# Kernel tuning notes

Hardware: AMD Instinct MI355X
Metric: run time of the kernel (lower is better)

Reference implementation:

```python
import jax, jax.numpy as jnp
import numpy as np

B, T, D = 2, 2048, 2048
H, DH = 16, 128
FG = 5461
EPS = 1e-5
ROPE_BASE = 10000.0


def rmsnorm(x, w):
    rms = jax.lax.rsqrt(jnp.mean(x * x, axis=-1, keepdims=True) + EPS)
    return x * rms * w


def rotate_half(x):
    x1 = x[..., ::2]
    x2 = x[..., 1::2]
    return jnp.stack((-x2, x1), axis=-1).reshape(x.shape)


def rope_tables(t_len, dh, dtype):
    inv_freq = 1.0 / (ROPE_BASE ** (np.arange(0, dh, 2, dtype=np.float32) / dh))
    t = np.arange(t_len, dtype=np.float32)
    freqs = np.outer(t, inv_freq)                 # [T, dh/2]
    emb = np.repeat(freqs, 2, axis=-1)            # repeat_interleave -> [T, dh]
    return jnp.asarray(np.cos(emb), dtype), jnp.asarray(np.sin(emb), dtype)


def setup_inputs() -> dict:
    key = jax.random.key(0)
    ks = jax.random.split(key, 8)
    s_attn = 1.0 / np.sqrt(D)
    s_gate = 1.0 / np.sqrt(D)
    s_proj = 1.0 / np.sqrt(FG)
    return {
        "x": jax.random.normal(ks[0], (B, T, D), jnp.float32),
        "norm1_w": jnp.ones((D,), jnp.float32),
        "norm2_w": jnp.ones((D,), jnp.float32),
        "c_attn_w": jax.random.normal(ks[1], (3 * D, D), jnp.float32) * s_attn,
        "c_proj_w": jax.random.normal(ks[2], (D, D), jnp.float32) * s_attn,
        "c_gate_w": jax.random.normal(ks[3], (FG, D), jnp.float32) * s_gate,
        "c_val_w": jax.random.normal(ks[4], (FG, D), jnp.float32) * s_gate,
        "c_mlp_proj_w": jax.random.normal(ks[5], (D, FG), jnp.float32) * s_proj,
    }


def block(x, norm1_w, norm2_w, c_attn_w, c_proj_w, c_gate_w, c_val_w, c_mlp_proj_w):
    # ---- attention branch (pre-norm) ----
    h = rmsnorm(x, norm1_w)
    qkv = h @ c_attn_w.T                                   # [B,T,3D]
    qkv = qkv.reshape(B, T, 3, H, DH).transpose(2, 0, 3, 1, 4)
    q, k, v = qkv[0], qkv[1], qkv[2]                       # [B,H,T,DH]
    cos, sin = rope_tables(T, DH, x.dtype)                 # [T,DH]
    q = q * cos + rotate_half(q) * sin
    k = k * cos + rotate_half(k) * sin
    att = jnp.einsum("bhqd,bhkd->bhqk", q, k) * (1.0 / np.sqrt(DH))
    causal = jnp.tril(jnp.ones((T, T), bool))
    att = jnp.where(causal, att, -jnp.inf)
    att = jax.nn.softmax(att, axis=-1)
    y = jnp.einsum("bhqk,bhkd->bhqd", att, v)              # [B,H,T,DH]
    y = y.transpose(0, 2, 1, 3).reshape(B, T, D)
    x = x + y @ c_proj_w.T
    # ---- MLP branch (pre-norm, SwiGLU) ----
    h = rmsnorm(x, norm2_w)
    gate = jax.nn.silu(h @ c_gate_w.T)                     # [B,T,FG]
    val = h @ c_val_w.T
    x = x + (gate * val) @ c_mlp_proj_w.T
    return x


def reference(x, norm1_w, norm2_w, c_attn_w, c_proj_w, c_gate_w, c_val_w, c_mlp_proj_w):
    return block(x, norm1_w, norm2_w, c_attn_w, c_proj_w, c_gate_w, c_val_w, c_mlp_proj_w)
```

## Files before the change

### kernel.cpp

```cpp
#include <hip/hip_runtime.h>
#include <hip/hip_bf16.h>
#include <stdint.h>

typedef __bf16 bf16_t;
typedef __bf16 bf16x8 __attribute__((ext_vector_type(8)));
typedef float  f32x4  __attribute__((ext_vector_type(4)));

#define DEV __device__ __forceinline__

constexpr int   Bn = 2, Tn = 2048, Dn = 2048, Hn = 16, DHn = 128;
constexpr int   BTn = Bn * Tn;
constexpr int   TD3 = 3 * Dn;
constexpr int   FGn = 5461, FGPn = 5504;
constexpr float EPSf   = 1e-5f;
constexpr float LOG2E  = 1.4426950408889634f;
constexpr float ASCALE = 0.08838834764831845f;
constexpr float LN1E4  = 9.210340371976184f;

DEV void gld16(void* lds, const void* g) {
  __builtin_amdgcn_global_load_lds(
      (__attribute__((address_space(1))) void*)(void*)g,
      (__attribute__((address_space(3))) void*)lds, 16, 0, 0);
}

DEV bf16x8 dsr128(const bf16_t* p) {
  bf16x8 r;
  asm volatile("ds_read_b128 %0, %1"
               : "=v"(r)
               : "v"((const __attribute__((address_space(3))) bf16_t*)p));
  return r;
}

__global__ __launch_bounds__(256)
void rmsnorm_k(const float* __restrict__ x, const float* __restrict__ w,
               bf16_t* __restrict__ out) {
  const int row = blockIdx.x;
  const int tid = threadIdx.x;
  const float* xr = x + (size_t)row * Dn;
  float4 a = ((const float4*)xr)[tid * 2];
  float4 b = ((const float4*)xr)[tid * 2 + 1];
  float ss = a.x*a.x + a.y*a.y + a.z*a.z + a.w*a.w
           + b.x*b.x + b.y*b.y + b.z*b.z + b.w*b.w;
#pragma unroll
  for (int off = 32; off > 0; off >>= 1) ss += __shfl_xor(ss, off, 64);
  __shared__ float red[4];
  if ((tid & 63) == 0) red[tid >> 6] = ss;
  __syncthreads();
  float tot = red[0] + red[1] + red[2] + red[3];
  float rms = rsqrtf(tot * (1.0f / Dn) + EPSf);
  float4 wa = ((const float4*)w)[tid * 2];
  float4 wb = ((const float4*)w)[tid * 2 + 1];
  bf16x8 o;
  o[0] = (bf16_t)(a.x * rms * wa.x); o[1] = (bf16_t)(a.y * rms * wa.y);
  o[2] = (bf16_t)(a.z * rms * wa.z); o[3] = (bf16_t)(a.w * rms * wa.w);
  o[4] = (bf16_t)(b.x * rms * wb.x); o[5] = (bf16_t)(b.y * rms * wb.y);
  o[6] = (bf16_t)(b.z * rms * wb.z); o[7] = (bf16_t)(b.w * rms * wb.w);
  *(bf16x8*)&out[(size_t)row * Dn + tid * 8] = o;
}

__global__ __launch_bounds__(256)
void cvt_pad_k(const float* __restrict__ src, bf16_t* __restrict__ dst,
               int srcR, int srcC, int dstC, int n8) {
  int i = blockIdx.x * 256 + threadIdx.x;
  if (i >= n8) return;
  long base = (long)i * 8;
  int r = (int)(base / dstC);
  int c = (int)(base % dstC);
  bf16x8 o;
#pragma unroll
  for (int k = 0; k < 8; ++k) {
    int cc = c + k;
    float v = (r < srcR && cc < srcC) ? src[(size_t)r * srcC + cc] : 0.0f;
    o[k] = (bf16_t)v;
  }
  *(bf16x8*)&dst[base] = o;
}

__global__ __launch_bounds__(256)
void reduce_k(float* __restrict__ out, const bf16_t* __restrict__ P0,
              const bf16_t* __restrict__ P1) {
  int i = blockIdx.x * 256 + threadIdx.x;
  bf16x8 p0 = *(const bf16x8*)&P0[(size_t)i * 8];
  bf16x8 p1 = *(const bf16x8*)&P1[(size_t)i * 8];
  float4 o0 = ((const float4*)out)[i * 2];
  float4 o1 = ((const float4*)out)[i * 2 + 1];
  o0.x += (float)p0[0] + (float)p1[0];
  o0.y += (float)p0[1] + (float)p1[1];
  o0.z += (float)p0[2] + (float)p1[2];
  o0.w += (float)p0[3] + (float)p1[3];
  o1.x += (float)p0[4] + (float)p1[4];
  o1.y += (float)p0[5] + (float)p1[5];
  o1.z += (float)p0[6] + (float)p1[6];
  o1.w += (float)p0[7] + (float)p1[7];
  ((float4*)out)[i * 2]     = o0;
  ((float4*)out)[i * 2 + 1] = o1;
}

template<int EPI>
__global__ __launch_bounds__(512, 2)
void gemm256(const bf16_t* __restrict__ A, const bf16_t* __restrict__ W,
             void* Cp, const void* Ep, int M, int N, int K, int ldc, int nby) {
  __shared__ __align__(128) bf16_t As[4][256 * 32];
  __shared__ __align__(128) bf16_t Bs[4][256 * 32];
  const int tid = threadIdx.x;
  const int lane = tid & 63, w = tid >> 6;
  const int wm = w >> 2, wn = w & 3;
  const int g = lane >> 4, q = lane & 15;

  const int nwg = gridDim.x;
  const int cpx = nwg >> 3;
  const int nid = (blockIdx.x & 7) * cpx + (blockIdx.x >> 3);
  const int bx = nid / nby, by = nid % nby;
  const int row0 = by * 256, col0 = bx * 256;

  f32x4 acc[8][4] = {};

  const bf16_t* Asrc[2];
  const bf16_t* Wsrc[2];
  int aoff[2];
#pragma unroll
  for (int i = 0; i < 2; ++i) {
    int line = i * 64 + (tid >> 3);
    int val  = (tid & 7) ^ (line & 7);
    int r    = (val >> 2) * 128 + line;
    int c    = val & 3;
    Asrc[i] = A + (size_t)(row0 + r) * K + c * 8;
    Wsrc[i] = W + (size_t)(col0 + r) * K + c * 8;
    aoff[i] = i * 8192 + w * 1024;
  }

  int offA[8], offB[4];
#pragma unroll
  for (int m = 0; m < 8; ++m) {
    int r = wm * 128 + m * 16 + q;
    offA[m] = (r & 127) * 128 + ((((r >> 7) * 4 + g) ^ (r & 7)) * 16);
  }
#pragma unroll
  for (int n = 0; n < 4; ++n) {
    int r = wn * 64 + n * 16 + q;
    offB[n] = (r & 127) * 128 + ((((r >> 7) * 4 + g) ^ (r & 7)) * 16);
  }

  const int NT = K >> 5;
  auto stage_full = [&](int T) {
    const int slot = T & 3, kk = T * 32;
#pragma unroll
    for (int i = 0; i < 2; ++i) {
      gld16((char*)As[slot] + aoff[i], Asrc[i] + kk);
      gld16((char*)Bs[slot] + aoff[i], Wsrc[i] + kk);
    }
  };

  bf16x8 af[8], bfr[4];

  auto step = [&](int T, bool do_stage, int waitsel) {
    const char* as_ = (const char*)As[T & 3];
    const char* bs_ = (const char*)Bs[T & 3];
#pragma unroll
    for (int m = 0; m < 8; ++m) af[m] = dsr128((const bf16_t*)(as_ + offA[m]));
#pragma unroll
    for (int n = 0; n < 4; ++n) bfr[n] = dsr128((const bf16_t*)(bs_ + offB[n]));
    if (do_stage) stage_full(T + 3);
    asm volatile("s_waitcnt lgkmcnt(0)" ::: "memory");
    __builtin_amdgcn_sched_barrier(0);
    __builtin_amdgcn_s_setprio(1);
#pragma unroll
    for (int m = 0; m < 8; ++m)
#pragma unroll
      for (int n = 0; n < 4; ++n)
        acc[m][n] = __builtin_amdgcn_mfma_f32_16x16x32_bf16(af[m], bfr[n], acc[m][n], 0, 0, 0);
    __builtin_amdgcn_s_setprio(0);
    __builtin_amdgcn_sched_barrier(0);
    if (waitsel == 2)      asm volatile("s_waitcnt vmcnt(8)" ::: "memory");
    else if (waitsel == 1) asm volatile("s_waitcnt vmcnt(4)" ::: "memory");
    else if (waitsel == 0) asm volatile("s_waitcnt vmcnt(0)" ::: "memory");
    asm volatile("s_barrier" ::: "memory");
  };

  stage_full(0); stage_full(1); stage_full(2);
  asm volatile("s_waitcnt vmcnt(8)" ::: "memory");
  asm volatile("s_barrier" ::: "memory");

  for (int T = 0; T < NT - 3; ++T) step(T, true, 2);
  step(NT - 3, false, 1);
  step(NT - 2, false, 0);
  step(NT - 1, false, 3);

#pragma unroll
  for (int m = 0; m < 8; ++m) {
#pragma unroll
    for (int n = 0; n < 4; ++n) {
#pragma unroll
      for (int j = 0; j < 4; ++j) {
        int r = row0 + wm * 128 + m * 16 + g * 4 + j;
        int c = col0 + wn * 64 + n * 16 + q;
        size_t idx = (size_t)r * ldc + c;
        float v = acc[m][n][j];
        if (EPI == 0) ((bf16_t*)Cp)[idx] = (bf16_t)v;
        else          ((float*)Cp)[idx] = ((const float*)Ep)[idx] + v;
      }
    }
  }
}

__global__ __launch_bounds__(512, 2)
void gemm_sk(const bf16_t* __restrict__ A, const bf16_t* __restrict__ W,
             bf16_t* __restrict__ P0, bf16_t* __restrict__ P1,
             int ldk, int klen, int ldc) {
  __shared__ __align__(128) bf16_t As[2][256 * 64];
  __shared__ __align__(128) bf16_t Bs[2][256 * 64];
  const int tid = threadIdx.x;
  const int lane = tid & 63, w = tid >> 6;
  const int wm = w >> 2, wn = w & 3;
  const int g = lane >> 4, q = lane & 15;

  const int nid = (blockIdx.x & 7) * 32 + (blockIdx.x >> 3);
  const int s   = nid >> 7;
  const int rem = nid & 127;
  const int bx = rem >> 4, by = rem & 15;
  const int row0 = by * 256, col0 = bx * 256;
  const int kofs = s * klen;
  bf16_t* P = s ? P1 : P0;

  f32x4 acc[8][4] = {};

  const bf16_t* Asrc[4];
  const bf16_t* Wsrc[4];
  int aoff[4];
#pragma unroll
  for (int i = 0; i < 4; ++i) {
    int ci = i * 512 + tid;
    int r  = ci >> 3;
    int cs = (ci & 7) ^ (r & 7);
    Asrc[i] = A + (size_t)(row0 + r) * ldk + kofs + cs * 8;
    Wsrc[i] = W + (size_t)(col0 + r) * ldk + kofs + cs * 8;
    aoff[i] = i * 8192 + w * 1024;
  }

  int offA[2][8], offB[2][4];
#pragma unroll
  for (int kk = 0; kk < 2; ++kk) {
#pragma unroll
    for (int m = 0; m < 8; ++m) {
      int r = wm * 128 + m * 16 + q;
      offA[kk][m] = r * 128 + (((kk * 4 + g) ^ (r & 7)) * 16);
    }
#pragma unroll
    for (int n = 0; n < 4; ++n) {
      int r = wn * 64 + n * 16 + q;
      offB[kk][n] = r * 128 + (((kk * 4 + g) ^ (r & 7)) * 16);
    }
  }

  const int NT = klen >> 6;
  auto stage = [&](int T, int h) {
    const int slot = T & 1;
    const size_t kk = (size_t)T * 64;
#pragma unroll
    for (int i = 0; i < 2; ++i) {
      int rd = h * 2 + i;
      gld16((char*)As[slot] + aoff[rd], Asrc[rd] + kk);
      gld16((char*)Bs[slot] + aoff[rd], Wsrc[rd] + kk);
    }
  };

  bf16x8 af[8], bfr[4];

  auto half = [&](const char* as_, const char* bs_, int kk) {
#pragma unroll
    for (int m = 0; m < 8; ++m) af[m] = dsr128((const bf16_t*)(as_ + offA[kk][m]));
#pragma unroll
    for (int n = 0; n < 4; ++n) bfr[n] = dsr128((const bf16_t*)(bs_ + offB[kk][n]));
  };
  auto mfmas = [&]() {
    asm volatile("s_waitcnt lgkmcnt(0)" ::: "memory");
    __builtin_amdgcn_sched_barrier(0);
    __builtin_amdgcn_s_setprio(1);
#pragma unroll
    for (int m = 0; m < 8; ++m)
#pragma unroll
      for (int n = 0; n < 4; ++n)
        acc[m][n] = __builtin_amdgcn_mfma_f32_16x16x32_bf16(af[m], bfr[n], acc[m][n], 0, 0, 0);
    __builtin_amdgcn_s_setprio(0);
    __builtin_amdgcn_sched_barrier(0);
  };

  stage(0, 0); stage(0, 1);
  asm volatile("s_waitcnt vmcnt(0)" ::: "memory");
  asm volatile("s_barrier" ::: "memory");

  for (int T = 0; T < NT; ++T) {
    const char* as_ = (const char*)As[T & 1];
    const char* bs_ = (const char*)Bs[T & 1];
    const bool st = (T + 1 < NT);
    half(as_, bs_, 0);
    if (st) stage(T + 1, 0);
    mfmas();
    half(as_, bs_, 1);
    if (st) stage(T + 1, 1);
    mfmas();
    if (st) asm volatile("s_waitcnt vmcnt(0)" ::: "memory");
    asm volatile("s_barrier" ::: "memory");
  }

#pragma unroll
  for (int m = 0; m < 8; ++m)
#pragma unroll
    for (int n = 0; n < 4; ++n)
#pragma unroll
      for (int j = 0; j < 4; ++j) {
        int r = row0 + wm * 128 + m * 16 + g * 4 + j;
        int c = col0 + wn * 64 + n * 16 + q;
        P[(size_t)r * ldc + c] = (bf16_t)acc[m][n][j];
      }
}

__global__ __launch_bounds__(512, 2)
void gemmgv(const bf16_t* __restrict__ A, const bf16_t* __restrict__ Wg,
            const bf16_t* __restrict__ Wv, bf16_t* __restrict__ Out,
            int M, int N, int K, int ldc, int nby) {
  __shared__ __align__(128) bf16_t As[2][256 * 32];
  __shared__ __align__(128) bf16_t Gs[2][128 * 32];
  __shared__ __align__(128) bf16_t Vs[2][128 * 32];
  const int tid = threadIdx.x;
  const int lane = tid & 63, w = tid >> 6;
  const int wm = w >> 2, wn = w & 3;
  const int g = lane >> 4, q = lane & 15;

  const int nwg = gridDim.x;
  const int cpx = nwg >> 3;
  const int nid = (blockIdx.x & 7) * cpx + (blockIdx.x >> 3);
  const int bx = nid / nby, by = nid % nby;
  const int row0 = by * 256, col0 = bx * 128;

  f32x4 accg[8][2] = {}, accv[8][2] = {};

  const bf16_t* Asrc[2];
  int aoff[2];
#pragma unroll
  for (int i = 0; i < 2; ++i) {
    int line = i * 64 + (tid >> 3);
    int val  = (tid & 7) ^ (line & 7);
    int r    = (val >> 2) * 128 + line;
    int c    = val & 3;
    Asrc[i] = A + (size_t)(row0 + r) * K + c * 8;
    aoff[i] = i * 8192 + w * 1024;
  }
  const int brow = tid >> 2;
  const int bchk = (tid & 3) ^ ((brow >> 1) & 3);
  const bf16_t* Gsrc = Wg + (size_t)(col0 + brow) * K + bchk * 8;
  const bf16_t* Vsrc = Wv + (size_t)(col0 + brow) * K + bchk * 8;
  const int boff = tid * 16;

  int offA[8], offB[2];
#pragma unroll
  for (int m = 0; m < 8; ++m) {
    int r = wm * 128 + m * 16 + q;
    offA[m] = (r & 127) * 128 + ((((r >> 7) * 4 + g) ^ (r & 7)) * 16);
  }
#pragma unroll
  for (int n = 0; n < 2; ++n) {
    int r = wn * 32 + n * 16 + q;
    offB[n] = r * 64 + ((g ^ ((r >> 1) & 3)) * 16);
  }

  const int NT = K >> 5;
  auto stage = [&](int T) {
    const int slot = T & 1, kk = T * 32;
    gld16((char*)As[slot] + aoff[0], Asrc[0] + kk);
    gld16((char*)As[slot] + aoff[1], Asrc[1] + kk);
    gld16((char*)Gs[slot] + boff, Gsrc + kk);
    gld16((char*)Vs[slot] + boff, Vsrc + kk);
  };

  stage(0);
  for (int T = 0; T < NT; ++T) {
    __syncthreads();
    if (T + 1 < NT) stage(T + 1);
    const char* as_ = (const char*)As[T & 1];
    const char* gs_ = (const char*)Gs[T & 1];
    const char* vs_ = (const char*)Vs[T & 1];
    bf16x8 af[8], bg[2], bv[2];
#pragma unroll
    for (int m = 0; m < 8; ++m) af[m] = *(const bf16x8*)(as_ + offA[m]);
#pragma unroll
    for (int n = 0; n < 2; ++n) {
      bg[n] = *(const bf16x8*)(gs_ + offB[n]);
      bv[n] = *(const bf16x8*)(vs_ + offB[n]);
    }
    __builtin_amdgcn_s_setprio(1);
#pragma unroll
    for (int m = 0; m < 8; ++m)
#pragma unroll
      for (int n = 0; n < 2; ++n) {
        accg[m][n] = __builtin_amdgcn_mfma_f32_16x16x32_bf16(af[m], bg[n], accg[m][n], 0, 0, 0);
        accv[m][n] = __builtin_amdgcn_mfma_f32_16x16x32_bf16(af[m], bv[n], accv[m][n], 0, 0, 0);
      }
    __builtin_amdgcn_s_setprio(0);
    __syncthreads();
  }

#pragma unroll
  for (int m = 0; m < 8; ++m) {
#pragma unroll
    for (int n = 0; n < 2; ++n) {
#pragma unroll
      for (int j = 0; j < 4; ++j) {
        int r = row0 + wm * 128 + m * 16 + g * 4 + j;
        int c = col0 + wn * 32 + n * 16 + q;
        float gt = accg[m][n][j];
        float sg = gt / (1.0f + __expf(-gt));
        Out[(size_t)r * ldc + c] = (bf16_t)(sg * accv[m][n][j]);
      }
    }
  }
}

__global__ __launch_bounds__(256)
void rope_k(const bf16_t* __restrict__ qkv, bf16_t* __restrict__ Qb,
            bf16_t* __restrict__ Kb, bf16_t* __restrict__ Vt) {
  const int t0 = blockIdx.x * 32;
  const int bh = blockIdx.y;
  const int b = bh >> 4, hh = bh & 15;
  __shared__ bf16_t Vl[32][132];

#pragma unroll
  for (int it = 0; it < 2; ++it) {
    int task = threadIdx.x + it * 256;
    int tt = task >> 4, ck = task & 15, d0 = ck * 8;
    int tg = t0 + tt;
    const bf16_t* srow = qkv + (size_t)(b * Tn + tg) * TD3 + hh * DHn + d0;
    bf16x8 qv = *(const bf16x8*)(srow);
    bf16x8 kv = *(const bf16x8*)(srow + Dn);
    bf16x8 vv = *(const bf16x8*)(srow + 2 * Dn);
    bf16x8 qo, ko;
#pragma unroll
    for (int p = 0; p < 4; ++p) {
      int jj = (d0 >> 1) + p;
      float fr = __expf(-((float)(2 * jj) / 128.0f) * LN1E4);
      float ang = (float)tg * fr;
      float cs = cosf(ang), sn = sinf(ang);
      float qe = (float)qv[2 * p], qod = (float)qv[2 * p + 1];
      float ke = (float)kv[2 * p], kod = (float)kv[2 * p + 1];
      qo[2 * p]     = (bf16_t)((qe * cs - qod * sn) * ASCALE);
      qo[2 * p + 1] = (bf16_t)((qod * cs + qe * sn) * ASCALE);
      ko[2 * p]     = (bf16_t)(ke * cs - kod * sn);
      ko[2 * p + 1] = (bf16_t)(kod * cs + ke * sn);
    }
    *(bf16x8*)&Qb[((size_t)bh * Tn + tg) * DHn + d0] = qo;
    *(bf16x8*)&Kb[((size_t)bh * Tn + tg) * DHn + d0] = ko;
    *(bf16x8*)&Vl[tt][d0] = vv;
  }
  __syncthreads();
#pragma unroll
  for (int it = 0; it < 2; ++it) {
    int task = threadIdx.x + it * 256;
    int dd = task >> 2, tc = (task & 3) * 8;
    bf16x8 ov;
#pragma unroll
    for (int i = 0; i < 8; ++i) ov[i] = Vl[tc + i][dd];
    *(bf16x8*)&Vt[((size_t)bh * DHn + dd) * Tn + t0 + tc] = ov;
  }
}

__global__ __launch_bounds__(256, 2)
void attn_k(const bf16_t* __restrict__ Qb, const bf16_t* __restrict__ Kb,
            const bf16_t* __restrict__ Vt, bf16_t* __restrict__ Y) {
  const int orig = blockIdx.x + 16 * blockIdx.y;
  const int nid  = (orig & 7) * 64 + (orig >> 3);
  const int pi = nid & 15;
  const int bh = nid >> 4;
  const int b = bh >> 4, hh = bh & 15;
  const int tid = threadIdx.x, lane = tid & 63, w = tid >> 6;
  const int g = lane >> 4, q = lane & 15;
  const int iA = pi, iB = 31 - pi;
  const int kmax = iB;

  __shared__ bf16_t Ks[2][64 * 128];
  __shared__ bf16_t Vs[2][128 * 64];
  __shared__ bf16_t Ps[4][16 * 72];

  bf16x8 aqA[4], aqB[4];
  {
    const bf16_t* QrA = Qb + ((size_t)bh * Tn + iA * 64 + w * 16 + q) * DHn;
    const bf16_t* QrB = Qb + ((size_t)bh * Tn + iB * 64 + w * 16 + q) * DHn;
#pragma unroll
    for (int s = 0; s < 4; ++s) {
      aqA[s] = *(const bf16x8*)(QrA + s * 32 + g * 8);
      aqB[s] = *(const bf16x8*)(QrB + s * 32 + g * 8);
    }
  }

  f32x4 oA[8] = {}, oB[8] = {};
  float mA[4], lA[4], mB[4], lB[4];
#pragma unroll
  for (int j = 0; j < 4; ++j) {
    mA[j] = -__builtin_inff(); lA[j] = 0.0f;
    mB[j] = -__builtin_inff(); lB[j] = 0.0f;
  }

  auto stage = [&](int buf, int kt) {
    const int k0 = kt * 64;
#pragma unroll
    for (int l = 0; l < 4; ++l) {
      int ci = (w * 4 + l) * 64 + lane;
      int kr = ci >> 4, kc = (ci & 15) ^ (kr & 7);
      gld16((char*)Ks[buf] + (w * 4 + l) * 1024,
            Kb + ((size_t)bh * Tn + k0 + kr) * DHn + kc * 8);
      int vr = ci >> 3, vc = (ci & 7) ^ (vr & 7);
      gld16((char*)Vs[buf] + (w * 4 + l) * 1024,
            Vt + ((size_t)bh * DHn + vr) * Tn + k0 + vc * 8);
    }
  };

  stage(0, 0);

  for (int kt = 0; kt <= kmax; ++kt) {
    __syncthreads();
    if (kt < kmax) stage((kt + 1) & 1, kt + 1);
    const bf16_t* ks = Ks[kt & 1];
    const bf16_t* vs = Vs[kt & 1];
    const bool actA = (kt <= iA);
    const int k0 = kt * 64;

    f32x4 saA[4] = {}, saB[4] = {};
    __builtin_amdgcn_s_setprio(1);
    if (actA) {
#pragma unroll
      for (int s = 0; s < 4; ++s) {
#pragma unroll
        for (int n = 0; n < 4; ++n) {
          bf16x8 bk = *(const bf16x8*)&ks[(n * 16 + q) * 128 + (((s * 4 + g) ^ (q & 7)) * 8)];
          saA[n] = __builtin_amdgcn_mfma_f32_16x16x32_bf16(aqA[s], bk, saA[n], 0, 0, 0);
          saB[n] = __builtin_amdgcn_mfma_f32_16x16x32_bf16(aqB[s], bk, saB[n], 0, 0, 0);
        }
      }
    } else {
#pragma unroll
      for (int s = 0; s < 4; ++s) {
#pragma unroll
        for (int n = 0; n < 4; ++n) {
          bf16x8 bk = *(const bf16x8*)&ks[(n * 16 + q) * 128 + (((s * 4 + g) ^ (q & 7)) * 8)];
          saB[n] = __builtin_amdgcn_mfma_f32_16x16x32_bf16(aqB[s], bk, saB[n], 0, 0, 0);
        }
      }
    }
    __builtin_amdgcn_s_setprio(0);

    bf16x8 paA[2], paB[2];
    auto softmax_p = [&](f32x4* sa, float* mst, float* lst, int itile,
                         bf16x8* pa, int qrow) {
      if (kt == itile) {
#pragma unroll
        for (int n = 0; n < 4; ++n)
#pragma unroll
          for (int j = 0; j < 4; ++j) {
            int kc = k0 + n * 16 + q;
            int qr = qrow + g * 4 + j;
            if (kc > qr) sa[n][j] = -1e30f;
          }
      }
      float mx[4];
#pragma unroll
      for (int j = 0; j < 4; ++j) {
        mx[j] = fmaxf(fmaxf(sa[0][j], sa[1][j]), fmaxf(sa[2][j], sa[3][j]));
#pragma unroll
        for (int off = 1; off < 16; off <<= 1)
          mx[j] = fmaxf(mx[j], __shfl_xor(mx[j], off, 16));
      }
      float ps[4][4], rsum[4];
#pragma unroll
      for (int j = 0; j < 4; ++j) rsum[j] = 0.0f;
      float mnew[4], corr[4];
#pragma unroll
      for (int j = 0; j < 4; ++j) {
        mnew[j] = fmaxf(mst[j], mx[j]);
        corr[j] = exp2f((mst[j] - mnew[j]) * LOG2E);
      }
#pragma unroll
      for (int n = 0; n < 4; ++n)
#pragma unroll
        for (int j = 0; j < 4; ++j) {
          ps[n][j] = exp2f((sa[n][j] - mnew[j]) * LOG2E);
          rsum[j] += ps[n][j];
        }
#pragma unroll
      for (int j = 0; j < 4; ++j) {
#pragma unroll
        for (int off = 1; off < 16; off <<= 1)
          rsum[j] += __shfl_xor(rsum[j], off, 16);
        lst[j] = lst[j] * corr[j] + rsum[j];
        mst[j] = mnew[j];
      }
#pragma unroll
      for (int n = 0; n < 4; ++n)
#pragma unroll
        for (int j = 0; j < 4; ++j)
          Ps[w][(g * 4 + j) * 72 + n * 16 + q] = (bf16_t)ps[n][j];
#pragma unroll
      for (int s2 = 0; s2 < 2; ++s2)
        pa[s2] = *(const bf16x8*)&Ps[w][q * 72 + s2 * 32 + g * 8];
      return corr;
    };

    float cA[4], cB[4];
    if (actA) {
      auto c = softmax_p(saA, mA, lA, iA, paA, iA * 64 + w * 16);
#pragma unroll
      for (int j = 0; j < 4; ++j) cA[j] = c[j];
#pragma unroll
      for (int n8 = 0; n8 < 8; ++n8)
#pragma unroll
        for (int j = 0; j < 4; ++j) oA[n8][j] *= cA[j];
    }
    {
      auto c = softmax_p(saB, mB, lB, iB, paB, iB * 64 + w * 16);
#pragma unroll
      for (int j = 0; j < 4; ++j) cB[j] = c[j];
#pragma unroll
      for (int n8 = 0; n8 < 8; ++n8)
#pragma unroll
        for (int j = 0; j < 4; ++j) oB[n8][j] *= cB[j];
    }

    __builtin_amdgcn_s_setprio(1);
    if (actA) {
#pragma unroll
      for (int s2 = 0; s2 < 2; ++s2)
#pragma unroll
        for (int n8 = 0; n8 < 8; ++n8) {
          bf16x8 bv = *(const bf16x8*)&vs[(n8 * 16 + q) * 64 + (((s2 * 4 + g) ^ (q & 7)) * 8)];
          oA[n8] = __builtin_amdgcn_mfma_f32_16x16x32_bf16(paA[s2], bv, oA[n8], 0, 0, 0);
          oB[n8] = __builtin_amdgcn_mfma_f32_16x16x32_bf16(paB[s2], bv, oB[n8], 0, 0, 0);
        }
    } else {
#pragma unroll
      for (int s2 = 0; s2 < 2; ++s2)
#pragma unroll
        for (int n8 = 0; n8 < 8; ++n8) {
          bf16x8 bv = *(const bf16x8*)&vs[(n8 * 16 + q) * 64 + (((s2 * 4 + g) ^ (q & 7)) * 8)];
          oB[n8] = __builtin_amdgcn_mfma_f32_16x16x32_bf16(paB[s2], bv, oB[n8], 0, 0, 0);
        }
    }
    __builtin_amdgcn_s_setprio(0);
  }

#pragma unroll
  for (int n8 = 0; n8 < 8; ++n8)
#pragma unroll
    for (int j = 0; j < 4; ++j) {
      int trA = iA * 64 + w * 16 + g * 4 + j;
      int trB = iB * 64 + w * 16 + g * 4 + j;
      Y[(size_t)(b * Tn + trA) * Dn + hh * DHn + n8 * 16 + q] =
          (bf16_t)(oA[n8][j] / lA[j]);
      Y[(size_t)(b * Tn + trB) * Dn + hh * DHn + n8 * 16 + q] =
          (bf16_t)(oB[n8][j] / lB[j]);
    }
}

extern "C" void kernel_launch(void* const* d_in, const int* in_sizes, int n_in,
                              void* d_out, int out_size, void* d_ws, size_t ws_size,
                              hipStream_t stream) {
  const float* x      = (const float*)d_in[0];
  const float* n1w    = (const float*)d_in[1];
  const float* n2w    = (const float*)d_in[2];
  const float* attn_w = (const float*)d_in[3];
  const float* proj_w = (const float*)d_in[4];
  const float* gate_w = (const float*)d_in[5];
  const float* val_w  = (const float*)d_in[6];
  const float* mlp_w  = (const float*)d_in[7];

  char* ws = (char*)d_ws;
  bf16_t* h    = (bf16_t*)(ws);
  bf16_t* bufA = (bf16_t*)(ws + 16777216);
  bf16_t* bufB = (bf16_t*)(ws + 67108864);
  bf16_t* wb   = (bf16_t*)(ws + 117440512);

  bf16_t* qkv  = bufA;
  bf16_t* wbV  = bufA;
  bf16_t* Qb   = bufB;
  bf16_t* Kb   = Qb + (size_t)32 * Tn * DHn;
  bf16_t* Vt   = Kb + (size_t)32 * Tn * DHn;
  bf16_t* gv   = bufB;
  bf16_t* y    = h;
  bf16_t* P0   = h;
  bf16_t* P1   = bufA;
  float*  out  = (float*)d_out;

  rmsnorm_k<<<BTn, 256, 0, stream>>>(x, n1w, h);
  cvt_pad_k<<<(TD3 * Dn / 8 + 255) / 256, 256, 0, stream>>>(attn_w, wb, TD3, Dn, Dn, TD3 * Dn / 8);
  gemm256<0><<<(TD3 / 256) * (BTn / 256), 512, 0, stream>>>(h, wb, (void*)qkv, nullptr, BTn, TD3, Dn, TD3, BTn / 256);
  rope_k<<<dim3(Tn / 32, 32), 256, 0, stream>>>(qkv, Qb, Kb, Vt);
  attn_k<<<dim3(16, 32), 256, 0, stream>>>(Qb, Kb, Vt, y);
  cvt_pad_k<<<(Dn * Dn / 8 + 255) / 256, 256, 0, stream>>>(proj_w, wb, Dn, Dn, Dn, Dn * Dn / 8);
  gemm256<1><<<(Dn / 256) * (BTn / 256), 512, 0, stream>>>(y, wb, (void*)out, (const void*)x, BTn, Dn, Dn, Dn, BTn / 256);
  rmsnorm_k<<<BTn, 256, 0, stream>>>(out, n2w, h);
  cvt_pad_k<<<(FGPn * Dn / 8 + 255) / 256, 256, 0, stream>>>(gate_w, wb, FGn, Dn, Dn, FGPn * Dn / 8);
  cvt_pad_k<<<(FGPn * Dn / 8 + 255) / 256, 256, 0, stream>>>(val_w, wbV, FGn, Dn, Dn, FGPn * Dn / 8);
  gemmgv<<<(FGPn / 128) * (BTn / 256), 512, 0, stream>>>(h, wb, wbV, gv, BTn, FGPn, Dn, FGPn, BTn / 256);
  cvt_pad_k<<<(Dn * FGPn / 8 + 255) / 256, 256, 0, stream>>>(mlp_w, wb, Dn, FGn, FGPn, Dn * FGPn / 8);
  gemm_sk<<<256, 512, 0, stream>>>(gv, wb, P0, P1, FGPn, FGPn / 2, Dn);
  reduce_k<<<BTn * Dn / 8 / 256, 256, 0, stream>>>(out, P0, P1);
}
```

Before: 814.7 us.

## Replace QKV and proj GEMMs with split-K kernel; retile gate/val GEMM to K=64

Removes gemm256 and runs the QKV and output-projection GEMMs through the split-K gemm_sk kernel, generalised to arbitrary grid sizes. New reduce kernels sum the two partials: one writes bf16 qkv, the other adds the residual and writes fp32 output. The gate/value GEMM moves to 64-wide K tiles with swizzled LDS loads, split-half staging, and explicit waitcnt/barrier pipelining in place of __syncthreads. The aim is more workgroups in flight for the smaller GEMMs and better load/MFMA overlap in gemmgv. The cost is extra partial-buffer traffic, two additional reduce launches, and bf16 rounding of the partial sums.

```diff
diff --git a/kernel.cpp b/kernel.cpp
--- a/kernel.cpp
+++ b/kernel.cpp
@@ -96,117 +96,43 @@
   ((float4*)out)[i * 2 + 1] = o1;
 }
 
-template<int EPI>
-__global__ __launch_bounds__(512, 2)
-void gemm256(const bf16_t* __restrict__ A, const bf16_t* __restrict__ W,
-             void* Cp, const void* Ep, int M, int N, int K, int ldc, int nby) {
-  __shared__ __align__(128) bf16_t As[4][256 * 32];
-  __shared__ __align__(128) bf16_t Bs[4][256 * 32];
-  const int tid = threadIdx.x;
-  const int lane = tid & 63, w = tid >> 6;
-  const int wm = w >> 2, wn = w & 3;
-  const int g = lane >> 4, q = lane & 15;
-
-  const int nwg = gridDim.x;
-  const int cpx = nwg >> 3;
-  const int nid = (blockIdx.x & 7) * cpx + (blockIdx.x >> 3);
-  const int bx = nid / nby, by = nid % nby;
-  const int row0 = by * 256, col0 = bx * 256;
-
-  f32x4 acc[8][4] = {};
-
-  const bf16_t* Asrc[2];
-  const bf16_t* Wsrc[2];
-  int aoff[2];
-#pragma unroll
-  for (int i = 0; i < 2; ++i) {
-    int line = i * 64 + (tid >> 3);
-    int val  = (tid & 7) ^ (line & 7);
-    int r    = (val >> 2) * 128 + line;
-    int c    = val & 3;
-    Asrc[i] = A + (size_t)(row0 + r) * K + c * 8;
-    Wsrc[i] = W + (size_t)(col0 + r) * K + c * 8;
-    aoff[i] = i * 8192 + w * 1024;
-  }
-
-  int offA[8], offB[4];
-#pragma unroll
-  for (int m = 0; m < 8; ++m) {
-    int r = wm * 128 + m * 16 + q;
-    offA[m] = (r & 127) * 128 + ((((r >> 7) * 4 + g) ^ (r & 7)) * 16);
-  }
-#pragma unroll
-  for (int n = 0; n < 4; ++n) {
-    int r = wn * 64 + n * 16 + q;
-    offB[n] = (r & 127) * 128 + ((((r >> 7) * 4 + g) ^ (r & 7)) * 16);
-  }
-
-  const int NT = K >> 5;
-  auto stage_full = [&](int T) {
-    const int slot = T & 3, kk = T * 32;
-#pragma unroll
-    for (int i = 0; i < 2; ++i) {
-      gld16((char*)As[slot] + aoff[i], Asrc[i] + kk);
-      gld16((char*)Bs[slot] + aoff[i], Wsrc[i] + kk);
-    }
-  };
-
-  bf16x8 af[8], bfr[4];
-
-  auto step = [&](int T, bool do_stage, int waitsel) {
-    const char* as_ = (const char*)As[T & 3];
-    const char* bs_ = (const char*)Bs[T & 3];
-#pragma unroll
-    for (int m = 0; m < 8; ++m) af[m] = dsr128((const bf16_t*)(as_ + offA[m]));
-#pragma unroll
-    for (int n = 0; n < 4; ++n) bfr[n] = dsr128((const bf16_t*)(bs_ + offB[n]));
-    if (do_stage) stage_full(T + 3);
-    asm volatile("s_waitcnt lgkmcnt(0)" ::: "memory");
-    __builtin_amdgcn_sched_barrier(0);
-    __builtin_amdgcn_s_setprio(1);
-#pragma unroll
-    for (int m = 0; m < 8; ++m)
-#pragma unroll
-      for (int n = 0; n < 4; ++n)
-        acc[m][n] = __builtin_amdgcn_mfma_f32_16x16x32_bf16(af[m], bfr[n], acc[m][n], 0, 0, 0);
-    __builtin_amdgcn_s_setprio(0);
-    __builtin_amdgcn_sched_barrier(0);
-    if (waitsel == 2)      asm volatile("s_waitcnt vmcnt(8)" ::: "memory");
-    else if (waitsel == 1) asm volatile("s_waitcnt vmcnt(4)" ::: "memory");
-    else if (waitsel == 0) asm volatile("s_waitcnt vmcnt(0)" ::: "memory");
-    asm volatile("s_barrier" ::: "memory");
-  };
-
-  stage_full(0); stage_full(1); stage_full(2);
-  asm volatile("s_waitcnt vmcnt(8)" ::: "memory");
-  asm volatile("s_barrier" ::: "memory");
-
-  for (int T = 0; T < NT - 3; ++T) step(T, true, 2);
-  step(NT - 3, false, 1);
-  step(NT - 2, false, 0);
-  step(NT - 1, false, 3);
-
-#pragma unroll
-  for (int m = 0; m < 8; ++m) {
-#pragma unroll
-    for (int n = 0; n < 4; ++n) {
-#pragma unroll
-      for (int j = 0; j < 4; ++j) {
-        int r = row0 + wm * 128 + m * 16 + g * 4 + j;
-        int c = col0 + wn * 64 + n * 16 + q;
-        size_t idx = (size_t)r * ldc + c;
-        float v = acc[m][n][j];
-        if (EPI == 0) ((bf16_t*)Cp)[idx] = (bf16_t)v;
-        else          ((float*)Cp)[idx] = ((const float*)Ep)[idx] + v;
-      }
-    }
-  }
+__global__ __launch_bounds__(256)
+void reduce2e(float* __restrict__ out, const float* __restrict__ E,
+              const bf16_t* __restrict__ P0, const bf16_t* __restrict__ P1) {
+  int i = blockIdx.x * 256 + threadIdx.x;
+  bf16x8 p0 = *(const bf16x8*)&P0[(size_t)i * 8];
+  bf16x8 p1 = *(const bf16x8*)&P1[(size_t)i * 8];
+  float4 e0 = ((const float4*)E)[i * 2];
+  float4 e1 = ((const float4*)E)[i * 2 + 1];
+  float4 o0, o1;
+  o0.x = e0.x + (float)p0[0] + (float)p1[0];
+  o0.y = e0.y + (float)p0[1] + (float)p1[1];
+  o0.z = e0.z + (float)p0[2] + (float)p1[2];
+  o0.w = e0.w + (float)p0[3] + (float)p1[3];
+  o1.x = e1.x + (float)p0[4] + (float)p1[4];
+  o1.y = e1.y + (float)p0[5] + (float)p1[5];
+  o1.z = e1.z + (float)p0[6] + (float)p1[6];
+  o1.w = e1.w + (float)p0[7] + (float)p1[7];
+  ((float4*)out)[i * 2]     = o0;
+  ((float4*)out)[i * 2 + 1] = o1;
+}
+
+__global__ __launch_bounds__(256)
+void reduce2b(bf16_t* __restrict__ outb, const bf16_t* __restrict__ P0,
+              const bf16_t* __restrict__ P1) {
+  int i = blockIdx.x * 256 + threadIdx.x;
+  bf16x8 p0 = *(const bf16x8*)&P0[(size_t)i * 8];
+  bf16x8 p1 = *(const bf16x8*)&P1[(size_t)i * 8];
+  bf16x8 o;
+#pragma unroll
+  for (int k = 0; k < 8; ++k) o[k] = (bf16_t)((float)p0[k] + (float)p1[k]);
+  *(bf16x8*)&outb[(size_t)i * 8] = o;
 }
 
 __global__ __launch_bounds__(512, 2)
 void gemm_sk(const bf16_t* __restrict__ A, const bf16_t* __restrict__ W,
              bf16_t* __restrict__ P0, bf16_t* __restrict__ P1,
-             int ldk, int klen, int ldc) {
+             int ldk, int klen, int ldc, int nby) {
   __shared__ __align__(128) bf16_t As[2][256 * 64];
   __shared__ __align__(128) bf16_t Bs[2][256 * 64];
   const int tid = threadIdx.x;
@@ -214,10 +140,13 @@
   const int wm = w >> 2, wn = w & 3;
   const int g = lane >> 4, q = lane & 15;
 
-  const int nid = (blockIdx.x & 7) * 32 + (blockIdx.x >> 3);
-  const int s   = nid >> 7;
-  const int rem = nid & 127;
-  const int bx = rem >> 4, by = rem & 15;
+  const int nwg = gridDim.x;
+  const int cpx = nwg >> 3;
+  const int nid = (blockIdx.x & 7) * cpx + (blockIdx.x >> 3);
+  const int half = nwg >> 1;
+  const int s   = nid / half;
+  const int rem = nid % half;
+  const int bx = rem / nby, by = rem % nby;
   const int row0 = by * 256, col0 = bx * 256;
   const int kofs = s * klen;
   bf16_t* P = s ? P1 : P0;
@@ -266,7 +195,7 @@
 
   bf16x8 af[8], bfr[4];
 
-  auto half = [&](const char* as_, const char* bs_, int kk) {
+  auto half_rd = [&](const char* as_, const char* bs_, int kk) {
 #pragma unroll
     for (int m = 0; m < 8; ++m) af[m] = dsr128((const bf16_t*)(as_ + offA[kk][m]));
 #pragma unroll
@@ -293,10 +222,10 @@
     const char* as_ = (const char*)As[T & 1];
     const char* bs_ = (const char*)Bs[T & 1];
     const bool st = (T + 1 < NT);
-    half(as_, bs_, 0);
+    half_rd(as_, bs_, 0);
     if (st) stage(T + 1, 0);
     mfmas();
-    half(as_, bs_, 1);
+    half_rd(as_, bs_, 1);
     if (st) stage(T + 1, 1);
     mfmas();
     if (st) asm volatile("s_waitcnt vmcnt(0)" ::: "memory");
@@ -318,10 +247,10 @@
 __global__ __launch_bounds__(512, 2)
 void gemmgv(const bf16_t* __restrict__ A, const bf16_t* __restrict__ Wg,
             const bf16_t* __restrict__ Wv, bf16_t* __restrict__ Out,
-            int M, int N, int K, int ldc, int nby) {
-  __shared__ __align__(128) bf16_t As[2][256 * 32];
-  __shared__ __align__(128) bf16_t Gs[2][128 * 32];
-  __shared__ __align__(128) bf16_t Vs[2][128 * 32];
+            int K, int ldc, int nby) {
+  __shared__ __align__(128) bf16_t As[2][256 * 64];
+  __shared__ __align__(128) bf16_t Gs[2][128 * 64];
+  __shared__ __align__(128) bf16_t Vs[2][128 * 64];
   const int tid = threadIdx.x;
   const int lane = tid & 63, w = tid >> 6;
   const int wm = w >> 2, wn = w & 3;
@@ -335,69 +264,100 @@
 
   f32x4 accg[8][2] = {}, accv[8][2] = {};
 
-  const bf16_t* Asrc[2];
-  int aoff[2];
+  const bf16_t* Asrc[4];
+  int aoff[4];
+#pragma unroll
+  for (int i = 0; i < 4; ++i) {
+    int ci = i * 512 + tid;
+    int r  = ci >> 3;
+    int cs = (ci & 7) ^ (r & 7);
+    Asrc[i] = A + (size_t)(row0 + r) * K + cs * 8;
+    aoff[i] = i * 8192 + w * 1024;
+  }
+  const bf16_t* Gsrc[2];
+  const bf16_t* Vsrc[2];
+  int boff[2];
 #pragma unroll
   for (int i = 0; i < 2; ++i) {
-    int line = i * 64 + (tid >> 3);
-    int val  = (tid & 7) ^ (line & 7);
-    int r    = (val >> 2) * 128 + line;
-    int c    = val & 3;
-    Asrc[i] = A + (size_t)(row0 + r) * K + c * 8;
-    aoff[i] = i * 8192 + w * 1024;
-  }
-  const int brow = tid >> 2;
-  const int bchk = (tid & 3) ^ ((brow >> 1) & 3);
-  const bf16_t* Gsrc = Wg + (size_t)(col0 + brow) * K + bchk * 8;
-  const bf16_t* Vsrc = Wv + (size_t)(col0 + brow) * K + bchk * 8;
-  const int boff = tid * 16;
-
-  int offA[8], offB[2];
-#pragma unroll
-  for (int m = 0; m < 8; ++m) {
-    int r = wm * 128 + m * 16 + q;
-    offA[m] = (r & 127) * 128 + ((((r >> 7) * 4 + g) ^ (r & 7)) * 16);
-  }
-#pragma unroll
-  for (int n = 0; n < 2; ++n) {
-    int r = wn * 32 + n * 16 + q;
-    offB[n] = r * 64 + ((g ^ ((r >> 1) & 3)) * 16);
-  }
-
-  const int NT = K >> 5;
-  auto stage = [&](int T) {
-    const int slot = T & 1, kk = T * 32;
-    gld16((char*)As[slot] + aoff[0], Asrc[0] + kk);
-    gld16((char*)As[slot] + aoff[1], Asrc[1] + kk);
-    gld16((char*)Gs[slot] + boff, Gsrc + kk);
-    gld16((char*)Vs[slot] + boff, Vsrc + kk);
+    int ci = i * 512 + tid;
+    int r  = ci >> 3;
+    int cs = (ci & 7) ^ (r & 7);
+    Gsrc[i] = Wg + (size_t)(col0 + r) * K + cs * 8;
+    Vsrc[i] = Wv + (size_t)(col0 + r) * K + cs * 8;
+    boff[i] = i * 8192 + w * 1024;
+  }
+
+  int offA[2][8], offB[2][2];
+#pragma unroll
+  for (int kk = 0; kk < 2; ++kk) {
+#pragma unroll
+    for (int m = 0; m < 8; ++m) {
+      int r = wm * 128 + m * 16 + q;
+      offA[kk][m] = r * 128 + (((kk * 4 + g) ^ (r & 7)) * 16);
+    }
+#pragma unroll
+    for (int n = 0; n < 2; ++n) {
+      int r = wn * 32 + n * 16 + q;
+      offB[kk][n] = r * 128 + (((kk * 4 + g) ^ (r & 7)) * 16);
+    }
+  }
+
+  const int NT = K >> 6;
+  auto stage = [&](int T, int h) {
+    const int slot = T & 1;
+    const size_t kk = (size_t)T * 64;
+#pragma unroll
+    for (int i = 0; i < 2; ++i) {
+      int rd = h * 2 + i;
+      gld16((char*)As[slot] + aoff[rd], Asrc[rd] + kk);
+    }
+    gld16((char*)Gs[slot] + boff[h], Gsrc[h] + kk);
+    gld16((char*)Vs[slot] + boff[h], Vsrc[h] + kk);
   };
 
-  stage(0);
+  bf16x8 af[8], bg[2], bv[2];
+
+  auto half_rd = [&](const char* as_, const char* gs_, const char* vs_, int kk) {
+#pragma unroll
+    for (int m = 0; m < 8; ++m) af[m] = dsr128((const bf16_t*)(as_ + offA[kk][m]));
+#pragma unroll
+    for (int n = 0; n < 2; ++n) {
+      bg[n] = dsr128((const bf16_t*)(gs_ + offB[kk][n]));
+      bv[n] = dsr128((const bf16_t*)(vs_ + offB[kk][n]));
+    }
+  };
+  auto mfmas = [&]() {
+    asm volatile("s_waitcnt lgkmcnt(0)" ::: "memory");
+    __builtin_amdgcn_sched_barrier(0);
+    __builtin_amdgcn_s_setprio(1);
+#pragma unroll
+    for (int m = 0; m < 8; ++m)
+#pragma unroll
+      for (int n = 0; n < 2; ++n) {
+        accg[m][n] = __builtin_amdgcn_mfma_f32_16x16x32_bf16(af[m], bg[n], accg[m][n], 0, 0, 0);
+        accv[m][n] = __builtin_amdgcn_mfma_f32_16x16x32_bf16(af[m], bv[n], accv[m][n], 0, 0, 0);
+      }
+    __builtin_amdgcn_s_setprio(0);
+    __builtin_amdgcn_sched_barrier(0);
+  };
+
+  stage(0, 0); stage(0, 1);
+  asm volatile("s_waitcnt vmcnt(0)" ::: "memory");
+  asm volatile("s_barrier" ::: "memory");
+
   for (int T = 0; T < NT; ++T) {
-    __syncthreads();
-    if (T + 1 < NT) stage(T + 1);
     const char* as_ = (const char*)As[T & 1];
     const char* gs_ = (const char*)Gs[T & 1];
     const char* vs_ = (const char*)Vs[T & 1];
-    bf16x8 af[8], bg[2], bv[2];
-#pragma unroll
-    for (int m = 0; m < 8; ++m) af[m] = *(const bf16x8*)(as_ + offA[m]);
-#pragma unroll
-    for (int n = 0; n < 2; ++n) {
-      bg[n] = *(const bf16x8*)(gs_ + offB[n]);
-      bv[n] = *(const bf16x8*)(vs_ + offB[n]);
-    }
-    __builtin_amdgcn_s_setprio(1);
-#pragma unroll
-    for (int m = 0; m < 8; ++m)
-#pragma unroll
-      for (int n = 0; n < 2; ++n) {
-        accg[m][n] = __builtin_amdgcn_mfma_f32_16x16x32_bf16(af[m], bg[n], accg[m][n], 0, 0, 0);
-        accv[m][n] = __builtin_amdgcn_mfma_f32_16x16x32_bf16(af[m], bv[n], accv[m][n], 0, 0, 0);
-      }
-    __builtin_amdgcn_s_setprio(0);
-    __syncthreads();
+    const bool st = (T + 1 < NT);
+    half_rd(as_, gs_, vs_, 0);
+    if (st) stage(T + 1, 0);
+    mfmas();
+    half_rd(as_, gs_, vs_, 1);
+    if (st) stage(T + 1, 1);
+    mfmas();
+    if (st) asm volatile("s_waitcnt vmcnt(0)" ::: "memory");
+    asm volatile("s_barrier" ::: "memory");
   }
 
 #pragma unroll
@@ -676,29 +636,35 @@
   bf16_t* bufB = (bf16_t*)(ws + 67108864);
   bf16_t* wb   = (bf16_t*)(ws + 117440512);
 
+  bf16_t* Pq0  = bufB;
+  bf16_t* Pq1  = bufA;
   bf16_t* qkv  = bufA;
-  bf16_t* wbV  = bufA;
   bf16_t* Qb   = bufB;
   bf16_t* Kb   = Qb + (size_t)32 * Tn * DHn;
   bf16_t* Vt   = Kb + (size_t)32 * Tn * DHn;
+  bf16_t* y    = h;
+  bf16_t* Pp0  = bufA;
+  bf16_t* Pp1  = bufA + (size_t)BTn * Dn;
+  bf16_t* wbV  = bufA;
   bf16_t* gv   = bufB;
-  bf16_t* y    = h;
-  bf16_t* P0   = h;
-  bf16_t* P1   = bufA;
+  bf16_t* Pm0  = h;
+  bf16_t* Pm1  = bufA;
   float*  out  = (float*)d_out;
 
   rmsnorm_k<<<BTn, 256, 0, stream>>>(x, n1w, h);
   cvt_pad_k<<<(TD3 * Dn / 8 + 255) / 256, 256, 0, stream>>>(attn_w, wb, TD3, Dn, Dn, TD3 * Dn / 8);
-  gemm256<0><<<(TD3 / 256) * (BTn / 256), 512, 0, stream>>>(h, wb, (void*)qkv, nullptr, BTn, TD3, Dn, TD3, BTn / 256);
+  gemm_sk<<<768, 512, 0, stream>>>(h, wb, Pq0, Pq1, Dn, Dn / 2, TD3, BTn / 256);
+  reduce2b<<<BTn * TD3 / 8 / 256, 256, 0, stream>>>(qkv, Pq0, Pq1);
   rope_k<<<dim3(Tn / 32, 32), 256, 0, stream>>>(qkv, Qb, Kb, Vt);
   attn_k<<<dim3(16, 32), 256, 0, stream>>>(Qb, Kb, Vt, y);
   cvt_pad_k<<<(Dn * Dn / 8 + 255) / 256, 256, 0, stream>>>(proj_w, wb, Dn, Dn, Dn, Dn * Dn / 8);
-  gemm256<1><<<(Dn / 256) * (BTn / 256), 512, 0, stream>>>(y, wb, (void*)out, (const void*)x, BTn, Dn, Dn, Dn, BTn / 256);
+  gemm_sk<<<256, 512, 0, stream>>>(y, wb, Pp0, Pp1, Dn, Dn / 2, Dn, BTn / 256);
+  reduce2e<<<BTn * Dn / 8 / 256, 256, 0, stream>>>(out, x, Pp0, Pp1);
   rmsnorm_k<<<BTn, 256, 0, stream>>>(out, n2w, h);
   cvt_pad_k<<<(FGPn * Dn / 8 + 255) / 256, 256, 0, stream>>>(gate_w, wb, FGn, Dn, Dn, FGPn * Dn / 8);
   cvt_pad_k<<<(FGPn * Dn / 8 + 255) / 256, 256, 0, stream>>>(val_w, wbV, FGn, Dn, Dn, FGPn * Dn / 8);
-  gemmgv<<<(FGPn / 128) * (BTn / 256), 512, 0, stream>>>(h, wb, wbV, gv, BTn, FGPn, Dn, FGPn, BTn / 256);
+  gemmgv<<<(FGPn / 128) * (BTn / 256), 512, 0, stream>>>(h, wb, wbV, gv, Dn, FGPn, BTn / 256);
   cvt_pad_k<<<(Dn * FGPn / 8 + 255) / 256, 256, 0, stream>>>(mlp_w, wb, Dn, FGn, FGPn, Dn * FGPn / 8);
-  gemm_sk<<<256, 512, 0, stream>>>(gv, wb, P0, P1, FGPn, FGPn / 2, Dn);
-  reduce_k<<<BTn * Dn / 8 / 256, 256, 0, stream>>>(out, P0, P1);
-}
+  gemm_sk<<<256, 512, 0, stream>>>(gv, wb, Pm0, Pm1, FGPn, FGPn / 2, Dn, BTn / 256);
+  reduce_k<<<BTn * Dn / 8 / 256, 256, 0, stream>>>(out, Pm0, Pm1);
+}
```

Result: faster. 730.2 us (-10.4%).
